# Performance work log

Hardware: AMD Instinct MI355X
Metric: run time of the kernel (lower is better)

## Reference

```python
import jax, jax.numpy as jnp
import numpy as np

B, T, F, H = 64, 512, 132, 1024


def setup_inputs() -> dict:
    key = jax.random.key(0)
    ks = jax.random.split(key, 16)
    k = 1.0 / np.sqrt(H)
    u = lambda kk, shape: jax.random.uniform(kk, shape, jnp.float32, -k, k)
    return {
        "real_seq": jax.random.normal(ks[0], (B, T, F), jnp.float32),
        "Wih1": u(ks[1], (4 * H, F)), "Whh1": u(ks[2], (4 * H, H)),
        "bih1": u(ks[3], (4 * H,)), "bhh1": u(ks[4], (4 * H,)),
        "Wih2": u(ks[5], (4 * H, H)), "Whh2": u(ks[6], (4 * H, H)),
        "bih2": u(ks[7], (4 * H,)), "bhh2": u(ks[8], (4 * H,)),
        "Wih3": u(ks[9], (4 * H, H)), "Whh3": u(ks[10], (4 * H, H)),
        "bih3": u(ks[11], (4 * H,)), "bhh3": u(ks[12], (4 * H,)),
        "Wd": u(ks[13], (F, H)), "bd": u(ks[14], (F,)),
        "condition_num": 5, "groundtruth_num": 5,
    }


def _cell(x, h, c, Wih, Whh, bih, bhh):
    # torch LSTMCell gate order: i, f, g, o
    gates = x @ Wih.T + h @ Whh.T + bih + bhh
    i, f, g, o = jnp.split(gates, 4, axis=-1)
    c_new = jax.nn.sigmoid(f) * c + jax.nn.sigmoid(i) * jnp.tanh(g)
    h_new = jax.nn.sigmoid(o) * jnp.tanh(c_new)
    return h_new, c_new


def reference(real_seq, Wih1, Whh1, bih1, bhh1, Wih2, Whh2, bih2, bhh2,
              Wih3, Whh3, bih3, bhh3, Wd, bd, condition_num, groundtruth_num):
    batch, seq_len, _ = real_seq.shape
    hid = Whh1.shape[1]
    out_dim = Wd.shape[0]
    # static teacher-forcing schedule (numpy, as in get_condition_lst)
    gt = np.ones((100, groundtruth_num))
    con = np.zeros((100, condition_num))
    cond = jnp.asarray(np.concatenate((gt, con), 1).reshape(-1)[:seq_len],
                       jnp.float32)

    def step(carry, xs):
        h0, h1, h2, c0, c1, c2, prev_out = carry
        frame, flag = xs
        in_frame = jnp.where(flag == 1.0, frame, prev_out)
        # NOTE: faithful to source -- lstm2 gets OLD h0, lstm3 gets OLD h1
        h0n, c0n = _cell(in_frame, h0, c0, Wih1, Whh1, bih1, bhh1)
        h1n, c1n = _cell(h0, h1, c1, Wih2, Whh2, bih2, bhh2)
        h2n, c2n = _cell(h1, h2, c2, Wih3, Whh3, bih3, bhh3)
        out = h2n @ Wd.T + bd
        return (h0n, h1n, h2n, c0n, c1n, c2n, out), out

    z = jnp.zeros((batch, hid), real_seq.dtype)
    out0 = jnp.zeros((batch, out_dim), real_seq.dtype)
    _, outs = jax.lax.scan(step, (z, z, z, z, z, z, out0),
                           (jnp.swapaxes(real_seq, 0, 1), cond))
    # outs: [T, B, F] -> concat along feature axis per timestep: [B, T*F]
    return jnp.transpose(outs, (1, 0, 2)).reshape(batch, seq_len * out_dim)
```

## Files before the change

### kernel.cpp

```cpp
#include <hip/hip_runtime.h>
#include <cstdint>


#define NBLK 256
#define NTHR 512
#define Bn 64
#define Tn 512
#define Fn 132
#define Hn 1024
#define TF (Tn * Fn)
#define SRCH 65536
#define HBUF 196608
#define XTT 10240
#define WPB 102400

typedef _Float16 h8 __attribute__((ext_vector_type(8)));
typedef float f4 __attribute__((ext_vector_type(4)));

__device__ __forceinline__ float sigf(float x) { return 1.0f / (1.0f + expf(-x)); }

__device__ __forceinline__ h8 cload16(const _Float16* p) {
    union { unsigned long long u[2]; h8 v; } c;
    c.u[0] = __hip_atomic_load((unsigned long long*)p, __ATOMIC_RELAXED,
                               __HIP_MEMORY_SCOPE_AGENT);
    c.u[1] = __hip_atomic_load((unsigned long long*)p + 1, __ATOMIC_RELAXED,
                               __HIP_MEMORY_SCOPE_AGENT);
    return c.v;
}
__device__ __forceinline__ void cstore8(void* p, unsigned long long v) {
    __hip_atomic_store((unsigned long long*)p, v, __ATOMIC_RELAXED,
                       __HIP_MEMORY_SCOPE_AGENT);
}

__device__ __forceinline__ void gsyncA(unsigned* bar, unsigned ep) {
    __syncthreads();
    if (threadIdx.x == 0) {
        unsigned* cnt = bar + ((blockIdx.x >> 5) << 5);
        unsigned old = __hip_atomic_fetch_add(cnt, 1u, __ATOMIC_RELAXED,
                                              __HIP_MEMORY_SCOPE_AGENT);
        if (old == 32u * ep - 1u) {
            unsigned d = __hip_atomic_fetch_add(bar + 256, 1u, __ATOMIC_RELAXED,
                                                __HIP_MEMORY_SCOPE_AGENT);
            if (d == 8u * ep - 1u)
                __hip_atomic_store(bar + 288, ep, __ATOMIC_RELAXED,
                                   __HIP_MEMORY_SCOPE_AGENT);
        }
        while (__hip_atomic_load(bar + 288, __ATOMIC_RELAXED,
                                 __HIP_MEMORY_SCOPE_AGENT) < ep)
            __builtin_amdgcn_s_sleep(1);
    }
    __syncthreads();
}


__global__ void k_bsum(const float* bih1, const float* bhh1, const float* bih2,
                       const float* bhh2, const float* bih3, const float* bhh3,
                       const float* Wih1, const float* bd,
                       float* bsum, float* bsum2) {
    int i = blockIdx.x * 256 + threadIdx.x;
    if (i < NBLK * 48) {
        int bidw = i / 48, r = i % 48;
        int cell = r >> 4, n = r & 15;
        int row = (n >> 2) * Hn + bidw * 4 + (n & 3);
        const float* bi = cell == 0 ? bih1 : (cell == 1 ? bih2 : bih3);
        const float* bh = cell == 0 ? bhh1 : (cell == 1 ? bhh2 : bhh3);
        bsum[i] = bi[row] + bh[row];
    } else if (i < NBLK * 64) {
        int ii = i - NBLK * 48;
        int bidw = ii / 16, n = ii % 16;
        int row = (n >> 2) * Hn + bidw * 4 + (n & 3);
        float s = 0.0f;
        for (int f = 0; f < Fn; ++f) s += Wih1[(size_t)row * Fn + f] * bd[f];
        bsum2[bidw * 16 + n] = s;
    }
}

__global__ void k_convx(const float* xseq, _Float16* xT) {
    int i = blockIdx.x * 256 + threadIdx.x;
    if (i >= Tn * XTT) return;
    int t = i / XTT, r = i % XTT;
    int k8 = r >> 9, b = (r >> 3) & 63, e = r & 7;
    int f = k8 * 8 + e;
    float v = (f < Fn) ? xseq[((size_t)b * Tn + t) * Fn + f] : 0.0f;
    xT[i] = (_Float16)v;
}

__global__ void k_convw(const float* Wih1, const float* Whh1, const float* Wih2,
                        const float* Whh2, const float* Wih3, const float* Whh3,
                        const float* Wd, _Float16* wblob) {
    int i = blockIdx.x * 256 + threadIdx.x;
    if (i >= NBLK * WPB) return;
    int bidw = i / WPB, r = i % WPB;
    int slot = r >> 9, e = r & 511;
    int w = slot / 25, s = slot - w * 25;
    int l = e >> 3, j = e & 7;
    int kq = l >> 4, n = l & 15;
    int row = (n >> 2) * Hn + bidw * 4 + (n & 3);
    float v = 0.0f;
    if (s >= 21) {
        int kt = w * 4 + (s - 21);
        int k = kt * 32 + kq * 8 + j;
        float acc = 0.0f;
        for (int f = 0; f < Fn; ++f)
            acc += Wih1[(size_t)row * Fn + f] * Wd[(size_t)f * Hn + k];
        v = acc;
    } else {
        const float* M;
        int K, kt;
        if (s < 4)       { M = Whh1; K = Hn; kt = w * 4 + s; }
        else if (s < 8)  { M = Wih2; K = Hn; kt = w * 4 + s - 4; }
        else if (s < 12) { M = Whh2; K = Hn; kt = w * 4 + s - 8; }
        else if (s < 16) { M = Wih3; K = Hn; kt = w * 4 + s - 12; }
        else if (s < 20) { M = Whh3; K = Hn; kt = w * 4 + s - 16; }
        else             { M = Wih1; K = Fn; kt = w; }
        int k = kt * 32 + kq * 8 + j;
        if (!(s == 20 && w >= 5) && k < K) v = M[(size_t)row * K + k];
    }
    wblob[i] = (_Float16)v;
}

__global__ void k_misc(_Float16* hT) {
    int i = blockIdx.x * 256 + threadIdx.x;
    if (i < HBUF) hT[i] = (_Float16)0.0f;
}


__global__ __launch_bounds__(NTHR, 2) void lstm_mfma(
    const _Float16* __restrict__ xT, const _Float16* __restrict__ wblob,
    _Float16* __restrict__ hT, const float* __restrict__ bsum,
    const float* __restrict__ bsum2, const float* __restrict__ Wd,
    const float* __restrict__ bd, const int* __restrict__ cnum_p,
    const int* __restrict__ gnum_p, float* __restrict__ dout,
    unsigned* __restrict__ bar) {
    __shared__ float red[8 * 12 * 68 * 4];
    __shared__ float cst[768];
    __shared__ float sbias[48];
    __shared__ float sbias2[16];
    __shared__ unsigned long long hstage[192];

    const int tid = threadIdx.x;
    const int bid = blockIdx.x;
    const int lane = tid & 63;
    const int wid = tid >> 6;
    const int laneA0 = (lane >> 4) * 512 + (lane & 15) * 8;

    if (tid < 48) sbias[tid] = bsum[bid * 48 + tid];
    if (tid >= 64 && tid < 80) sbias2[tid - 64] = bsum2[bid * 16 + (tid - 64)];
    for (int i = tid; i < 768; i += NTHR) cst[i] = 0.0f;

    h8 wfr[25];
    {
        const _Float16* wp = wblob + (size_t)bid * WPB + (size_t)(wid * 25) * 512 + lane * 8;
#pragma unroll
        for (int s2 = 0; s2 < 25; ++s2) wfr[s2] = *(const h8*)(wp + s2 * 512);
    }
    __syncthreads();

    const int gnum = gnum_p[0];
    const int per = gnum + cnum_p[0];

    unsigned epA = 0;
    int tmod = 0;
    for (int t = 0; t < Tn; ++t) {
        const int flag = (tmod < gnum) ? 1 : 0;
        const bool fused = (!flag) && (t > 0);
        const int rb = t % 3, wb2 = (t + 1) % 3;
        const _Float16* hr = hT + (size_t)rb * HBUF;
        _Float16* hw = hT + (size_t)wb2 * HBUF;

        f4 acc[12];
#pragma unroll
        for (int i = 0; i < 12; ++i) acc[i] = (f4){0.f, 0.f, 0.f, 0.f};

        if (flag && wid < 5) {
            const _Float16* x0 = xT + (size_t)t * XTT + wid * 2048 + laneA0;
#pragma unroll
            for (int mt = 0; mt < 4; ++mt) {
                h8 a = *(const h8*)(x0 + mt * 128);
                acc[mt] = __builtin_amdgcn_mfma_f32_16x16x32_f16(a, wfr[20], acc[mt], 0, 0, 0);
            }
        }
        {
            const _Float16* s0 = hr + wid * 4 * 2048 + laneA0;
#pragma unroll
            for (int i2 = 0; i2 < 4; ++i2) {
#pragma unroll
                for (int mt = 0; mt < 4; ++mt) {
                    h8 a = cload16(s0 + i2 * 2048 + mt * 128);
                    acc[mt]     = __builtin_amdgcn_mfma_f32_16x16x32_f16(a, wfr[i2],     acc[mt],     0, 0, 0);
                    acc[4 + mt] = __builtin_amdgcn_mfma_f32_16x16x32_f16(a, wfr[4 + i2], acc[4 + mt], 0, 0, 0);
                }
            }
        }
        {
            const _Float16* s1 = hr + SRCH + wid * 4 * 2048 + laneA0;
#pragma unroll
            for (int i2 = 0; i2 < 4; ++i2) {
#pragma unroll
                for (int mt = 0; mt < 4; ++mt) {
                    h8 a = cload16(s1 + i2 * 2048 + mt * 128);
                    acc[4 + mt] = __builtin_amdgcn_mfma_f32_16x16x32_f16(a, wfr[8 + i2],  acc[4 + mt], 0, 0, 0);
                    acc[8 + mt] = __builtin_amdgcn_mfma_f32_16x16x32_f16(a, wfr[12 + i2], acc[8 + mt], 0, 0, 0);
                }
            }
        }
        {
            const _Float16* s2 = hr + 2 * SRCH + wid * 4 * 2048 + laneA0;
            if (fused) {
#pragma unroll
                for (int i2 = 0; i2 < 4; ++i2) {
#pragma unroll
                    for (int mt = 0; mt < 4; ++mt) {
                        h8 a = cload16(s2 + i2 * 2048 + mt * 128);
                        acc[8 + mt] = __builtin_amdgcn_mfma_f32_16x16x32_f16(a, wfr[16 + i2], acc[8 + mt], 0, 0, 0);
                        acc[mt]     = __builtin_amdgcn_mfma_f32_16x16x32_f16(a, wfr[21 + i2], acc[mt],     0, 0, 0);
                    }
                }
            } else {
#pragma unroll
                for (int i2 = 0; i2 < 4; ++i2) {
#pragma unroll
                    for (int mt = 0; mt < 4; ++mt) {
                        h8 a = cload16(s2 + i2 * 2048 + mt * 128);
                        acc[8 + mt] = __builtin_amdgcn_mfma_f32_16x16x32_f16(a, wfr[16 + i2], acc[8 + mt], 0, 0, 0);
                    }
                }
            }
        }

        {
            float* wr = red + ((size_t)(wid * 12) * 68 + (lane >> 4) * 17 + (lane & 15)) * 4;
#pragma unroll
            for (int cc = 0; cc < 3; ++cc)
#pragma unroll
                for (int mt = 0; mt < 4; ++mt)
                    *(f4*)(wr + (cc * 4 + mt) * 68 * 4) = acc[cc * 4 + mt];
        }
        __syncthreads();
        const float bmul = fused ? 1.0f : 0.0f;
        for (int idx = tid; idx < 768; idx += NTHR) {
            const int cell = idx >> 8, jj = (idx >> 6) & 3, b = idx & 63;
            const int mt = b >> 4, mq = (b >> 2) & 3, rr = b & 3;
            float gv4[4];
#pragma unroll
            for (int gt = 0; gt < 4; ++gt) {
                const int n = gt * 4 + jj;
                float v = sbias[cell * 16 + n];
                if (cell == 0) v += bmul * sbias2[n];
#pragma unroll
                for (int w2 = 0; w2 < 8; ++w2)
                    v += red[(((w2 * 12 + cell * 4 + mt)) * 68 + mq * 17 + n) * 4 + rr];
                gv4[gt] = v;
            }
            const float cold = cst[(cell * 4 + jj) * 64 + b];
            const float cn = sigf(gv4[1]) * cold + sigf(gv4[0]) * tanhf(gv4[2]);
            cst[(cell * 4 + jj) * 64 + b] = cn;
            const float hn = sigf(gv4[3]) * tanhf(cn);
            ((_Float16*)hstage)[(cell * 64 + b) * 4 + jj] = (_Float16)hn;
        }
        __syncthreads();
        if (tid < 192) {
            const int cell = tid >> 6, b = tid & 63;
            _Float16* dst = hw + cell * SRCH + (bid >> 1) * 512 + b * 8 + 4 * (bid & 1);
            cstore8(dst, hstage[tid]);
        }

        ++epA;
        gsyncA(bar, epA);

        {
            const _Float16* h2 = hT + (size_t)wb2 * HBUF + 2 * SRCH;
            const int ss = tid >> 6, b = tid & 63;
            const int nj = (bid < 8) ? 2 : 1;
            for (int j2 = 0; j2 < nj; ++j2) {
                int f, half;
                if (j2 == 0) {
                    if (bid < Fn) { f = bid; half = 0; }
                    else          { f = bid - Fn; half = 1; }
                } else { f = bid + (NBLK - Fn); half = 1; }
                const float* wdr = Wd + (size_t)f * Hn;
                float p = 0.0f;
#pragma unroll
                for (int i = 0; i < 8; ++i) {
                    const int k8 = half * 64 + ss * 8 + i;
                    h8 hv = cload16(h2 + k8 * 512 + b * 8);
                    const float4 w0 = *(const float4*)(wdr + k8 * 8);
                    const float4 w1 = *(const float4*)(wdr + k8 * 8 + 4);
                    p = fmaf((float)hv[0], w0.x, p); p = fmaf((float)hv[1], w0.y, p);
                    p = fmaf((float)hv[2], w0.z, p); p = fmaf((float)hv[3], w0.w, p);
                    p = fmaf((float)hv[4], w1.x, p); p = fmaf((float)hv[5], w1.y, p);
                    p = fmaf((float)hv[6], w1.z, p); p = fmaf((float)hv[7], w1.w, p);
                }
                red[ss * 64 + b] = p;
                __syncthreads();
                if (tid < 64) {
                    float o = (half == 0) ? bd[f] : 0.0f;
#pragma unroll
                    for (int u = 0; u < 8; ++u) o += red[u * 64 + tid];
                    unsafeAtomicAdd(&dout[(size_t)tid * TF + (size_t)t * Fn + f], o);
                }
                __syncthreads();
            }
        }
        tmod = (tmod + 1 >= per) ? 0 : (tmod + 1);
    }
}


extern "C" void kernel_launch(void* const* d_in, const int* in_sizes, int n_in,
                              void* d_out, int out_size, void* d_ws, size_t ws_size,
                              hipStream_t stream) {
    const float* xseq = (const float*)d_in[0];
    const float* Wih1 = (const float*)d_in[1];
    const float* Whh1 = (const float*)d_in[2];
    const float* bih1 = (const float*)d_in[3];
    const float* bhh1 = (const float*)d_in[4];
    const float* Wih2 = (const float*)d_in[5];
    const float* Whh2 = (const float*)d_in[6];
    const float* bih2 = (const float*)d_in[7];
    const float* bhh2 = (const float*)d_in[8];
    const float* Wih3 = (const float*)d_in[9];
    const float* Whh3 = (const float*)d_in[10];
    const float* bih3 = (const float*)d_in[11];
    const float* bhh3 = (const float*)d_in[12];
    const float* Wd = (const float*)d_in[13];
    const float* bd = (const float*)d_in[14];
    const int* cnum_p = (const int*)d_in[15];
    const int* gnum_p = (const int*)d_in[16];

    unsigned char* ws = (unsigned char*)d_ws;
    unsigned* bar = (unsigned*)ws;
    float* bsum = (float*)(ws + 4096);
    float* bsum2 = (float*)(ws + 53248);
    _Float16* xT = (_Float16*)(ws + 102400);
    _Float16* wblob = (_Float16*)(ws + 102400 + 10485760);
    _Float16* hT = (_Float16*)(ws + 102400 + 10485760 + 52428800);

    hipMemsetAsync(bar, 0, 4096, stream);
    hipMemsetAsync(d_out, 0, (size_t)out_size * sizeof(float), stream);
    hipLaunchKernelGGL(k_bsum, dim3((NBLK * 64 + 255) / 256), dim3(256), 0, stream,
                       bih1, bhh1, bih2, bhh2, bih3, bhh3, Wih1, bd, bsum, bsum2);
    hipLaunchKernelGGL(k_convx, dim3((Tn * XTT + 255) / 256), dim3(256), 0, stream,
                       xseq, xT);
    hipLaunchKernelGGL(k_convw, dim3((NBLK * WPB + 255) / 256), dim3(256), 0, stream,
                       Wih1, Whh1, Wih2, Whh2, Wih3, Whh3, Wd, wblob);
    hipLaunchKernelGGL(k_misc, dim3((HBUF + 255) / 256), dim3(256), 0, stream, hT);
    hipLaunchKernelGGL(lstm_mfma, dim3(NBLK), dim3(NTHR), 0, stream,
                       xT, wblob, hT, bsum, bsum2, Wd, bd, cnum_p, gnum_p,
                       (float*)d_out, bar);
}
```

Measured before the change: 8.587 ms.

## Stage hidden state per XCD and overlap decoder with global barrier

Each step, the blocks on an XCD cooperatively copy the hidden-state buffer into a per-XCD staging area and synchronize on a per-XCD counter. The MFMA A-operands are then read from that area with raw buffer loads, replacing agent-scope atomic loads. The global barrier is split into arrive and wait, and the output decoder for the previous step runs between them, hiding barrier latency. This adds an extra copy pass and an XCD-local sync each step, plus a trailing decoder for the last step.

```diff
diff --git a/kernel.cpp b/kernel.cpp
--- a/kernel.cpp
+++ b/kernel.cpp
@@ -13,42 +13,62 @@
 #define HBUF 196608
 #define XTT 10240
 #define WPB 102400
+#define STB 393216
+#define STU 49152
 
 typedef _Float16 h8 __attribute__((ext_vector_type(8)));
 typedef float f4 __attribute__((ext_vector_type(4)));
+typedef int v4i __attribute__((ext_vector_type(4)));
+typedef unsigned long long ull;
+
+__device__ v4i llvm_amdgcn_raw_buffer_load_v4i32(v4i srsrc, int voffset,
+                                                 int soffset, int aux)
+    __asm("llvm.amdgcn.raw.buffer.load.v4i32");
+
+__device__ __forceinline__ v4i make_srd(const void* p) {
+    union { struct { unsigned lo, hi, sz, cfg; } s; v4i v; } u;
+    u.s.lo = (unsigned)(uintptr_t)p;
+    u.s.hi = (unsigned)((uintptr_t)p >> 32);
+    u.s.sz = 0xFFFFFFFFu;
+    u.s.cfg = 0x00020000u;
+    return u.v;
+}
+
+__device__ __forceinline__ h8 bload16(v4i rsrc, int voff) {
+    union { v4i i; h8 h; } c;
+    c.i = llvm_amdgcn_raw_buffer_load_v4i32(rsrc, voff, 0, 1 );
+    return c.h;
+}
 
 __device__ __forceinline__ float sigf(float x) { return 1.0f / (1.0f + expf(-x)); }
 
-__device__ __forceinline__ h8 cload16(const _Float16* p) {
-    union { unsigned long long u[2]; h8 v; } c;
-    c.u[0] = __hip_atomic_load((unsigned long long*)p, __ATOMIC_RELAXED,
+__device__ __forceinline__ ull cload8(const void* p) {
+    return __hip_atomic_load((const ull*)p, __ATOMIC_RELAXED, __HIP_MEMORY_SCOPE_AGENT);
+}
+__device__ __forceinline__ void cstore8(void* p, ull v) {
+    __hip_atomic_store((ull*)p, v, __ATOMIC_RELAXED, __HIP_MEMORY_SCOPE_AGENT);
+}
+
+__device__ __forceinline__ void garrive(unsigned* bar, unsigned ep) {
+    unsigned* cnt = bar + ((blockIdx.x >> 5) << 5);
+    unsigned old = __hip_atomic_fetch_add(cnt, 1u, __ATOMIC_RELAXED,
+                                          __HIP_MEMORY_SCOPE_AGENT);
+    if (old == 32u * ep - 1u) {
+        unsigned d = __hip_atomic_fetch_add(bar + 256, 1u, __ATOMIC_RELAXED,
+                                            __HIP_MEMORY_SCOPE_AGENT);
+        if (d == 8u * ep - 1u)
+            __hip_atomic_store(bar + 288, ep, __ATOMIC_RELAXED,
                                __HIP_MEMORY_SCOPE_AGENT);
-    c.u[1] = __hip_atomic_load((unsigned long long*)p + 1, __ATOMIC_RELAXED,
-                               __HIP_MEMORY_SCOPE_AGENT);
-    return c.v;
-}
-__device__ __forceinline__ void cstore8(void* p, unsigned long long v) {
-    __hip_atomic_store((unsigned long long*)p, v, __ATOMIC_RELAXED,
-                       __HIP_MEMORY_SCOPE_AGENT);
-}
-
+    }
+}
+__device__ __forceinline__ void gwait(unsigned* bar, unsigned ep) {
+    while (__hip_atomic_load(bar + 288, __ATOMIC_RELAXED,
+                             __HIP_MEMORY_SCOPE_AGENT) < ep)
+        __builtin_amdgcn_s_sleep(1);
+}
 __device__ __forceinline__ void gsyncA(unsigned* bar, unsigned ep) {
     __syncthreads();
-    if (threadIdx.x == 0) {
-        unsigned* cnt = bar + ((blockIdx.x >> 5) << 5);
-        unsigned old = __hip_atomic_fetch_add(cnt, 1u, __ATOMIC_RELAXED,
-                                              __HIP_MEMORY_SCOPE_AGENT);
-        if (old == 32u * ep - 1u) {
-            unsigned d = __hip_atomic_fetch_add(bar + 256, 1u, __ATOMIC_RELAXED,
-                                                __HIP_MEMORY_SCOPE_AGENT);
-            if (d == 8u * ep - 1u)
-                __hip_atomic_store(bar + 288, ep, __ATOMIC_RELAXED,
-                                   __HIP_MEMORY_SCOPE_AGENT);
-        }
-        while (__hip_atomic_load(bar + 288, __ATOMIC_RELAXED,
-                                 __HIP_MEMORY_SCOPE_AGENT) < ep)
-            __builtin_amdgcn_s_sleep(1);
-    }
+    if (threadIdx.x == 0) { garrive(bar, ep); gwait(bar, ep); }
     __syncthreads();
 }
 
@@ -127,22 +147,25 @@
 
 __global__ __launch_bounds__(NTHR, 2) void lstm_mfma(
     const _Float16* __restrict__ xT, const _Float16* __restrict__ wblob,
-    _Float16* __restrict__ hT, const float* __restrict__ bsum,
-    const float* __restrict__ bsum2, const float* __restrict__ Wd,
-    const float* __restrict__ bd, const int* __restrict__ cnum_p,
-    const int* __restrict__ gnum_p, float* __restrict__ dout,
-    unsigned* __restrict__ bar) {
+    _Float16* __restrict__ hT, unsigned char* __restrict__ xstage,
+    const float* __restrict__ bsum, const float* __restrict__ bsum2,
+    const float* __restrict__ Wd, const float* __restrict__ bd,
+    const int* __restrict__ cnum_p, const int* __restrict__ gnum_p,
+    float* __restrict__ dout, unsigned* __restrict__ bar) {
     __shared__ float red[8 * 12 * 68 * 4];
     __shared__ float cst[768];
     __shared__ float sbias[48];
     __shared__ float sbias2[16];
     __shared__ unsigned long long hstage[192];
+    __shared__ int sxi[3];
 
     const int tid = threadIdx.x;
     const int bid = blockIdx.x;
     const int lane = tid & 63;
     const int wid = tid >> 6;
+    const int laneAB = (lane >> 4) * 1024 + (lane & 15) * 16;
     const int laneA0 = (lane >> 4) * 512 + (lane & 15) * 8;
+    const int widB = wid * 16384;
 
     if (tid < 48) sbias[tid] = bsum[bid * 48 + tid];
     if (tid >= 64 && tid < 80) sbias2[tid - 64] = bsum2[bid * 16 + (tid - 64)];
@@ -154,19 +177,91 @@
 #pragma unroll
         for (int s2 = 0; s2 < 25; ++s2) wfr[s2] = *(const h8*)(wp + s2 * 512);
     }
+
+    if (tid == 0) {
+        unsigned x;
+        asm volatile("s_getreg_b32 %0, hwreg(HW_REG_XCC_ID)" : "=s"(x));
+        x &= 7u;
+        unsigned r = __hip_atomic_fetch_add(bar + 384 + x * 16, 1u,
+                                            __ATOMIC_RELAXED, __HIP_MEMORY_SCOPE_AGENT);
+        sxi[0] = (int)x; sxi[1] = (int)r;
+    }
+    gsyncA(bar, 1);
+    if (tid == 0)
+        sxi[2] = (int)__hip_atomic_load(bar + 384 + sxi[0] * 16, __ATOMIC_RELAXED,
+                                        __HIP_MEMORY_SCOPE_AGENT);
     __syncthreads();
+    const int xcd = sxi[0], xrank = sxi[1], xN = sxi[2];
+    unsigned* xb = bar + 640 + xcd * 16;
+    unsigned char* xsb = xstage + (size_t)xcd * 2 * STB;
 
     const int gnum = gnum_p[0];
     const int per = gnum + cnum_p[0];
 
-    unsigned epA = 0;
+    auto decoder = [&](v4i rsrc, int tt) {
+        const int ss = tid >> 6, b = tid & 63;
+        const int nj = (bid < 8) ? 2 : 1;
+        for (int j2 = 0; j2 < nj; ++j2) {
+            int f, half;
+            if (j2 == 0) {
+                if (bid < Fn) { f = bid; half = 0; }
+                else          { f = bid - Fn; half = 1; }
+            } else { f = bid + (NBLK - Fn); half = 1; }
+            const float* wdr = Wd + (size_t)f * Hn;
+            float p = 0.0f;
+#pragma unroll
+            for (int i = 0; i < 8; ++i) {
+                const int k8 = half * 64 + ss * 8 + i;
+                h8 hv = bload16(rsrc, 262144 + k8 * 1024 + b * 16);
+                const float4 w0 = *(const float4*)(wdr + k8 * 8);
+                const float4 w1 = *(const float4*)(wdr + k8 * 8 + 4);
+                p = fmaf((float)hv[0], w0.x, p); p = fmaf((float)hv[1], w0.y, p);
+                p = fmaf((float)hv[2], w0.z, p); p = fmaf((float)hv[3], w0.w, p);
+                p = fmaf((float)hv[4], w1.x, p); p = fmaf((float)hv[5], w1.y, p);
+                p = fmaf((float)hv[6], w1.z, p); p = fmaf((float)hv[7], w1.w, p);
+            }
+            red[ss * 64 + b] = p;
+            __syncthreads();
+            if (tid < 64) {
+                float o = (half == 0) ? bd[f] : 0.0f;
+#pragma unroll
+                for (int u = 0; u < 8; ++u) o += red[u * 64 + tid];
+                unsafeAtomicAdd(&dout[(size_t)tid * TF + (size_t)tt * Fn + f], o);
+            }
+            __syncthreads();
+        }
+    };
+
+    auto stage = [&](int rbuf, int slot) {
+        const ull* src = (const ull*)(hT + (size_t)rbuf * HBUF);
+        ull* dst = (ull*)(xsb + (size_t)slot * STB);
+        for (int s2 = xrank; s2 < 32; s2 += xN) {
+            const int u = s2 * 1536 + tid;
+#pragma unroll
+            for (int q = 0; q < 3; ++q)
+                dst[u + q * 512] = cload8(src + u + q * 512);
+        }
+        __syncthreads();
+    };
+    auto xsync = [&](unsigned target) {
+        if (tid == 0) {
+            __hip_atomic_fetch_add(xb, 1u, __ATOMIC_RELAXED, __HIP_MEMORY_SCOPE_AGENT);
+            while (__hip_atomic_load(xb, __ATOMIC_RELAXED, __HIP_MEMORY_SCOPE_AGENT) < target)
+                __builtin_amdgcn_s_sleep(1);
+        }
+        __syncthreads();
+    };
+
     int tmod = 0;
     for (int t = 0; t < Tn; ++t) {
         const int flag = (tmod < gnum) ? 1 : 0;
         const bool fused = (!flag) && (t > 0);
         const int rb = t % 3, wb2 = (t + 1) % 3;
-        const _Float16* hr = hT + (size_t)rb * HBUF;
         _Float16* hw = hT + (size_t)wb2 * HBUF;
+
+        stage(rb, t & 1);
+        xsync((unsigned)(xN * (t + 1)));
+        const v4i rsrc = make_srd(xsb + (size_t)(t & 1) * STB);
 
         f4 acc[12];
 #pragma unroll
@@ -180,50 +275,41 @@
                 acc[mt] = __builtin_amdgcn_mfma_f32_16x16x32_f16(a, wfr[20], acc[mt], 0, 0, 0);
             }
         }
-        {
-            const _Float16* s0 = hr + wid * 4 * 2048 + laneA0;
+#pragma unroll
+        for (int i2 = 0; i2 < 4; ++i2) {
+#pragma unroll
+            for (int mt = 0; mt < 4; ++mt) {
+                h8 a = bload16(rsrc, widB + i2 * 4096 + mt * 256 + laneAB);
+                acc[mt]     = __builtin_amdgcn_mfma_f32_16x16x32_f16(a, wfr[i2],     acc[mt],     0, 0, 0);
+                acc[4 + mt] = __builtin_amdgcn_mfma_f32_16x16x32_f16(a, wfr[4 + i2], acc[4 + mt], 0, 0, 0);
+            }
+        }
+#pragma unroll
+        for (int i2 = 0; i2 < 4; ++i2) {
+#pragma unroll
+            for (int mt = 0; mt < 4; ++mt) {
+                h8 a = bload16(rsrc, 131072 + widB + i2 * 4096 + mt * 256 + laneAB);
+                acc[4 + mt] = __builtin_amdgcn_mfma_f32_16x16x32_f16(a, wfr[8 + i2],  acc[4 + mt], 0, 0, 0);
+                acc[8 + mt] = __builtin_amdgcn_mfma_f32_16x16x32_f16(a, wfr[12 + i2], acc[8 + mt], 0, 0, 0);
+            }
+        }
+        if (fused) {
 #pragma unroll
             for (int i2 = 0; i2 < 4; ++i2) {
 #pragma unroll
                 for (int mt = 0; mt < 4; ++mt) {
-                    h8 a = cload16(s0 + i2 * 2048 + mt * 128);
-                    acc[mt]     = __builtin_amdgcn_mfma_f32_16x16x32_f16(a, wfr[i2],     acc[mt],     0, 0, 0);
-                    acc[4 + mt] = __builtin_amdgcn_mfma_f32_16x16x32_f16(a, wfr[4 + i2], acc[4 + mt], 0, 0, 0);
+                    h8 a = bload16(rsrc, 262144 + widB + i2 * 4096 + mt * 256 + laneAB);
+                    acc[8 + mt] = __builtin_amdgcn_mfma_f32_16x16x32_f16(a, wfr[16 + i2], acc[8 + mt], 0, 0, 0);
+                    acc[mt]     = __builtin_amdgcn_mfma_f32_16x16x32_f16(a, wfr[21 + i2], acc[mt],     0, 0, 0);
                 }
             }
-        }
-        {
-            const _Float16* s1 = hr + SRCH + wid * 4 * 2048 + laneA0;
+        } else {
 #pragma unroll
             for (int i2 = 0; i2 < 4; ++i2) {
 #pragma unroll
                 for (int mt = 0; mt < 4; ++mt) {
-                    h8 a = cload16(s1 + i2 * 2048 + mt * 128);
-                    acc[4 + mt] = __builtin_amdgcn_mfma_f32_16x16x32_f16(a, wfr[8 + i2],  acc[4 + mt], 0, 0, 0);
-                    acc[8 + mt] = __builtin_amdgcn_mfma_f32_16x16x32_f16(a, wfr[12 + i2], acc[8 + mt], 0, 0, 0);
-                }
-            }
-        }
-        {
-            const _Float16* s2 = hr + 2 * SRCH + wid * 4 * 2048 + laneA0;
-            if (fused) {
-#pragma unroll
-                for (int i2 = 0; i2 < 4; ++i2) {
-#pragma unroll
-                    for (int mt = 0; mt < 4; ++mt) {
-                        h8 a = cload16(s2 + i2 * 2048 + mt * 128);
-                        acc[8 + mt] = __builtin_amdgcn_mfma_f32_16x16x32_f16(a, wfr[16 + i2], acc[8 + mt], 0, 0, 0);
-                        acc[mt]     = __builtin_amdgcn_mfma_f32_16x16x32_f16(a, wfr[21 + i2], acc[mt],     0, 0, 0);
-                    }
-                }
-            } else {
-#pragma unroll
-                for (int i2 = 0; i2 < 4; ++i2) {
-#pragma unroll
-                    for (int mt = 0; mt < 4; ++mt) {
-                        h8 a = cload16(s2 + i2 * 2048 + mt * 128);
-                        acc[8 + mt] = __builtin_amdgcn_mfma_f32_16x16x32_f16(a, wfr[16 + i2], acc[8 + mt], 0, 0, 0);
-                    }
+                    h8 a = bload16(rsrc, 262144 + widB + i2 * 4096 + mt * 256 + laneAB);
+                    acc[8 + mt] = __builtin_amdgcn_mfma_f32_16x16x32_f16(a, wfr[16 + i2], acc[8 + mt], 0, 0, 0);
                 }
             }
         }
@@ -265,45 +351,19 @@
             cstore8(dst, hstage[tid]);
         }
 
-        ++epA;
-        gsyncA(bar, epA);
-
-        {
-            const _Float16* h2 = hT + (size_t)wb2 * HBUF + 2 * SRCH;
-            const int ss = tid >> 6, b = tid & 63;
-            const int nj = (bid < 8) ? 2 : 1;
-            for (int j2 = 0; j2 < nj; ++j2) {
-                int f, half;
-                if (j2 == 0) {
-                    if (bid < Fn) { f = bid; half = 0; }
-                    else          { f = bid - Fn; half = 1; }
-                } else { f = bid + (NBLK - Fn); half = 1; }
-                const float* wdr = Wd + (size_t)f * Hn;
-                float p = 0.0f;
-#pragma unroll
-                for (int i = 0; i < 8; ++i) {
-                    const int k8 = half * 64 + ss * 8 + i;
-                    h8 hv = cload16(h2 + k8 * 512 + b * 8);
-                    const float4 w0 = *(const float4*)(wdr + k8 * 8);
-                    const float4 w1 = *(const float4*)(wdr + k8 * 8 + 4);
-                    p = fmaf((float)hv[0], w0.x, p); p = fmaf((float)hv[1], w0.y, p);
-                    p = fmaf((float)hv[2], w0.z, p); p = fmaf((float)hv[3], w0.w, p);
-                    p = fmaf((float)hv[4], w1.x, p); p = fmaf((float)hv[5], w1.y, p);
-                    p = fmaf((float)hv[6], w1.z, p); p = fmaf((float)hv[7], w1.w, p);
-                }
-                red[ss * 64 + b] = p;
-                __syncthreads();
-                if (tid < 64) {
-                    float o = (half == 0) ? bd[f] : 0.0f;
-#pragma unroll
-                    for (int u = 0; u < 8; ++u) o += red[u * 64 + tid];
-                    unsafeAtomicAdd(&dout[(size_t)tid * TF + (size_t)t * Fn + f], o);
-                }
-                __syncthreads();
-            }
-        }
+        __syncthreads();
+        if (tid == 0) garrive(bar, (unsigned)(t + 2));
+        if (t > 0) decoder(rsrc, t - 1);
+        __syncthreads();
+        if (tid == 0) gwait(bar, (unsigned)(t + 2));
+        __syncthreads();
+
         tmod = (tmod + 1 >= per) ? 0 : (tmod + 1);
     }
+
+    stage(Tn % 3, Tn & 1);
+    xsync((unsigned)(xN * (Tn + 1)));
+    decoder(make_srd(xsb + (size_t)(Tn & 1) * STB), Tn - 1);
 }
 
 
@@ -335,6 +395,7 @@
     _Float16* xT = (_Float16*)(ws + 102400);
     _Float16* wblob = (_Float16*)(ws + 102400 + 10485760);
     _Float16* hT = (_Float16*)(ws + 102400 + 10485760 + 52428800);
+    unsigned char* xstage = ws + 102400 + 10485760 + 52428800 + 1179648;
 
     hipMemsetAsync(bar, 0, 4096, stream);
     hipMemsetAsync(d_out, 0, (size_t)out_size * sizeof(float), stream);
@@ -346,6 +407,6 @@
                        Wih1, Whh1, Wih2, Whh2, Wih3, Whh3, Wd, wblob);
     hipLaunchKernelGGL(k_misc, dim3((HBUF + 255) / 256), dim3(256), 0, stream, hT);
     hipLaunchKernelGGL(lstm_mfma, dim3(NBLK), dim3(NTHR), 0, stream,
-                       xT, wblob, hT, bsum, bsum2, Wd, bd, cnum_p, gnum_p,
+                       xT, wblob, hT, xstage, bsum, bsum2, Wd, bd, cnum_p, gnum_p,
                        (float*)d_out, bar);
 }
```

New measurement: 7.701 ms. 10.3% less time.
